# Kernel tuning notes

Hardware: AMD Instinct MI355X
Metric: run time of the kernel (lower is better)

Reference implementation:

```python
import jax, jax.numpy as jnp
import numpy as np

B, N, H = 32, 1024, 256
ALPHA = 0.2  # leaky relu slope
NEG_INF = -1e12


def setup_inputs() -> dict:
    key = jax.random.key(0)
    k1, k2, k3, k4, k5, k6 = jax.random.split(key, 6)
    inp = jax.random.normal(k1, (B, N, H), dtype=jnp.float32)
    A = (jax.random.uniform(k2, (B, N, N)) < 0.05).astype(jnp.float32)
    l = jnp.sort(jax.random.randint(k3, (B, 2), 0, N), axis=1)
    # xavier-uniform(gain=1.414) approximated; exact init values are irrelevant for correctness
    lim_w = 1.414 * np.sqrt(6.0 / (H + H))
    W_i = jax.random.uniform(k4, (H, H), minval=-lim_w, maxval=lim_w, dtype=jnp.float32)
    W_c = jax.random.uniform(k5, (H, H), minval=-lim_w, maxval=lim_w, dtype=jnp.float32)
    lim_a = 1.414 * np.sqrt(6.0 / (2 * H + 1))
    a = jax.random.uniform(k6, (2 * H, 1), minval=-lim_a, maxval=lim_a, dtype=jnp.float32)
    return {"inp": inp, "A": A, "l": l, "W_i": W_i, "W_c": W_c, "a": a}


def reference(inp, A, l, W_i, W_c, a):
    # eval mode: dropout is identity (training=False)
    n = inp.shape[1]
    h = inp.shape[2]
    Wh_i = jnp.einsum('bnh,he->bne', inp, W_i)
    Wh_c = jnp.einsum('bnh,he->bne', inp, W_c)
    # vectorized replacement of the per-batch Wh[index][i:j] = Wh_i[index][i:j] loop
    idx = jnp.arange(n)
    sel = (idx[None, :] >= l[:, 0:1]) & (idx[None, :] < l[:, 1:2])  # [B,N]
    Wh = jnp.where(sel[:, :, None], Wh_i, Wh_c)
    # additive attention scores
    Wh1 = Wh @ a[:h, :]  # [B,N,1]
    Wh2 = Wh @ a[h:, :]  # [B,N,1]
    A_ = A + jnp.eye(n, dtype=A.dtype)
    e = jax.nn.leaky_relu((Wh1 + jnp.swapaxes(Wh2, 1, 2)) * A_, ALPHA)
    att = jnp.where(A_ > 0, e, NEG_INF)
    att = jax.nn.softmax(att, axis=2)
    h_prime = jnp.einsum('bnm,bme->bne', att, Wh)
    return jax.nn.elu(h_prime)  # concat=True
```

## Files before the change

### kernel.cpp

```cpp
#include <hip/hip_runtime.h>
#include <hip/hip_bf16.h>
#include <stdint.h>

#define B_ 32
#define N_ 1024
#define H_ 256
#define PF_PITCH 520

typedef short bf16x8 __attribute__((ext_vector_type(8)));
typedef float floatx4 __attribute__((ext_vector_type(4)));

__device__ inline unsigned short f2bs(float x) {
    __hip_bfloat16 h = __float2bfloat16(x);
    return __builtin_bit_cast(unsigned short, h);
}

__global__ __launch_bounds__(256)
void k_uvec(const float* __restrict__ Wi, const float* __restrict__ Wc,
            const float* __restrict__ a, float* __restrict__ U) {
    int k = blockIdx.x;
    int t = threadIdx.x;
    float wi = Wi[k * H_ + t];
    float wc = Wc[k * H_ + t];
    float a1 = a[t], a2 = a[H_ + t];
    float p0 = wi * a1, p1 = wc * a1, p2 = wi * a2, p3 = wc * a2;
    for (int off = 32; off; off >>= 1) {
        p0 += __shfl_xor(p0, off);
        p1 += __shfl_xor(p1, off);
        p2 += __shfl_xor(p2, off);
        p3 += __shfl_xor(p3, off);
    }
    __shared__ float red[4][4];
    int w = t >> 6;
    if ((t & 63) == 0) { red[w][0] = p0; red[w][1] = p1; red[w][2] = p2; red[w][3] = p3; }
    __syncthreads();
    if (t == 0) {
        U[0 * H_ + k] = red[0][0] + red[1][0] + red[2][0] + red[3][0];
        U[1 * H_ + k] = red[0][1] + red[1][1] + red[2][1] + red[3][1];
        U[2 * H_ + k] = red[0][2] + red[1][2] + red[2][2] + red[3][2];
        U[3 * H_ + k] = red[0][3] + red[1][3] + red[2][3] + red[3][3];
    }
}

__global__ __launch_bounds__(256)
void k_abits(const float* __restrict__ A, unsigned int* __restrict__ M) {
    int t = threadIdx.x, w = t >> 6, lane = t & 63;
    size_t row = blockIdx.x;
    const float* Ar = A + row * N_ + w * 256 + lane * 4;
    float4 v = *reinterpret_cast<const float4*>(Ar);
    unsigned long long b0 = __ballot(v.x > 0.f);
    unsigned long long b1 = __ballot(v.y > 0.f);
    unsigned long long b2 = __ballot(v.z > 0.f);
    unsigned long long b3 = __ballot(v.w > 0.f);
    if (lane == 0) {
        unsigned int* Mp = M + (row * 4 + w) * 8;
        uint4 v0 = {(unsigned int)b0, (unsigned int)(b0 >> 32),
                    (unsigned int)b1, (unsigned int)(b1 >> 32)};
        uint4 v1 = {(unsigned int)b2, (unsigned int)(b2 >> 32),
                    (unsigned int)b3, (unsigned int)(b3 >> 32)};
        *reinterpret_cast<uint4*>(Mp) = v0;
        *reinterpret_cast<uint4*>(Mp + 4) = v1;
    }
}

__global__ __launch_bounds__(256)
void k_prep(const float* __restrict__ Wi, const float* __restrict__ Wc,
            unsigned short* __restrict__ WtFi, unsigned short* __restrict__ WtFc) {
    __shared__ float tile[64][65];
    int mat = blockIdx.x >> 4;
    int tr = ((blockIdx.x >> 2) & 3) * 64;
    int tc = (blockIdx.x & 3) * 64;
    const float* W = mat ? Wc : Wi;
    unsigned short* WtF = mat ? WtFc : WtFi;
    int t = threadIdx.x;
    int rr = t >> 2, c4 = (t & 3) * 16;
    const float* src = W + (size_t)(tr + rr) * H_ + tc + c4;
#pragma unroll
    for (int j = 0; j < 4; ++j) {
        float4 v = *reinterpret_cast<const float4*>(src + j * 4);
        tile[rr][c4 + 4 * j + 0] = v.x;
        tile[rr][c4 + 4 * j + 1] = v.y;
        tile[rr][c4 + 4 * j + 2] = v.z;
        tile[rr][c4 + 4 * j + 3] = v.w;
    }
    __syncthreads();
#pragma unroll
    for (int h = 0; h < 2; ++h) {
        int s = h * 256 + t;
        int ksl = s >> 8;
        int cl  = (s >> 6) & 3;
        int ll  = s & 63;
        int m16v = ll & 15, quadv = ll >> 4;
        int nloc = cl * 16 + m16v;
        int kb = ksl * 32 + quadv * 8;
        unsigned int pk[4];
#pragma unroll
        for (int jj = 0; jj < 4; ++jj) {
            unsigned short lo = f2bs(tile[kb + 2 * jj][nloc]);
            unsigned short hi = f2bs(tile[kb + 2 * jj + 1][nloc]);
            pk[jj] = (unsigned int)lo | ((unsigned int)hi << 16);
        }
        int ksg = (tr >> 5) + ksl;
        int cg  = (tc >> 4) + cl;
        *reinterpret_cast<uint4*>(WtF + ((size_t)(ksg * 16 + cg) * 64 + ll) * 8) =
            *reinterpret_cast<uint4*>(pk);
    }
}

__global__ __launch_bounds__(256)
void k_gemm(const float* __restrict__ inp, const int* __restrict__ l,
            const unsigned short* __restrict__ WtFi, const unsigned short* __restrict__ WtFc,
            unsigned short* __restrict__ WhF, const float* __restrict__ U,
            float* __restrict__ Wh1, float* __restrict__ Wh2) {
    __shared__ unsigned short bbuf[2][4096];
    int blk = blockIdx.x;
    int b  = blk >> 5;
    int r0 = ((blk >> 1) & 15) * 64;
    int n0 = (blk & 1) * 128;
    int t = threadIdx.x;
    int w = t >> 6;
    int lane = t & 63;
    int quad = lane >> 4, m16 = lane & 15;
    int rowb = r0 + w * 16;

    int l0 = l[2 * b], l1 = l[2 * b + 1];
    bool allI = (l0 <= r0) && (r0 + 64 <= l1);
    bool allC = (l1 <= r0) || (l0 >= r0 + 64);
    int npass = (allI || allC) ? 1 : 2;

    int row = rowb + m16;
    bool sel = (row >= l0) && (row < l1);
    const float* xrow = inp + ((size_t)(b * N_ + row)) * H_;
    const float* u1 = U + (sel ? 0 : H_);
    const float* u2 = U + 2 * H_ + (sel ? 0 : H_);
    bool doWh = (n0 == 0);
    float d1 = 0.f, d2 = 0.f;

    unsigned short* fb = WhF + (size_t)b * (N_ * H_);
    int cb = n0 >> 4;

    int j0 = rowb + quad * 4;
    int ksO = j0 >> 5;
    int laneF = m16 + 16 * ((j0 & 31) >> 3);
    int jj0 = j0 & 7;

    for (int pass = 0; pass < npass; ++pass) {
        const unsigned short* WtF =
            (npass == 1) ? (allI ? WtFi : WtFc) : (pass == 0 ? WtFi : WtFc);
        const unsigned short* gbase = WtF + cb * 512;

        floatx4 acc[8];
#pragma unroll
        for (int c = 0; c < 8; ++c) acc[c] = (floatx4){0.f, 0.f, 0.f, 0.f};

        {
            uint4 v0 = *reinterpret_cast<const uint4*>(gbase + (size_t)t * 8);
            uint4 v1 = *reinterpret_cast<const uint4*>(gbase + (size_t)(256 + t) * 8);
            *reinterpret_cast<uint4*>(&bbuf[0][t * 8]) = v0;
            *reinterpret_cast<uint4*>(&bbuf[0][(256 + t) * 8]) = v1;
        }
        for (int ks = 0; ks < 8; ++ks) {
            __syncthreads();
            uint4 v0, v1;
            if (ks < 7) {
                v0 = *reinterpret_cast<const uint4*>(gbase + (size_t)(ks + 1) * 8192 + t * 8);
                v1 = *reinterpret_cast<const uint4*>(gbase + (size_t)(ks + 1) * 8192 + (256 + t) * 8);
            }
            const float4 xa = *reinterpret_cast<const float4*>(xrow + ks * 32 + quad * 8);
            const float4 xb = *reinterpret_cast<const float4*>(xrow + ks * 32 + quad * 8 + 4);
            if (pass == 0 && doWh) {
                const float4 ua = *reinterpret_cast<const float4*>(u1 + ks * 32 + quad * 8);
                const float4 ub = *reinterpret_cast<const float4*>(u1 + ks * 32 + quad * 8 + 4);
                const float4 va = *reinterpret_cast<const float4*>(u2 + ks * 32 + quad * 8);
                const float4 vb = *reinterpret_cast<const float4*>(u2 + ks * 32 + quad * 8 + 4);
                d1 += xa.x * ua.x + xa.y * ua.y + xa.z * ua.z + xa.w * ua.w
                    + xb.x * ub.x + xb.y * ub.y + xb.z * ub.z + xb.w * ub.w;
                d2 += xa.x * va.x + xa.y * va.y + xa.z * va.z + xa.w * va.w
                    + xb.x * vb.x + xb.y * vb.y + xb.z * vb.z + xb.w * vb.w;
            }
            unsigned int pk0 = (unsigned int)f2bs(xa.x) | ((unsigned int)f2bs(xa.y) << 16);
            unsigned int pk1 = (unsigned int)f2bs(xa.z) | ((unsigned int)f2bs(xa.w) << 16);
            unsigned int pk2 = (unsigned int)f2bs(xb.x) | ((unsigned int)f2bs(xb.y) << 16);
            unsigned int pk3 = (unsigned int)f2bs(xb.z) | ((unsigned int)f2bs(xb.w) << 16);
            uint4 apk = {pk0, pk1, pk2, pk3};
            bf16x8 af = __builtin_bit_cast(bf16x8, apk);

            const unsigned short* bptr = &bbuf[ks & 1][lane * 8];
#pragma unroll
            for (int c = 0; c < 8; ++c) {
                bf16x8 bfr = *reinterpret_cast<const bf16x8*>(bptr + c * 512);
                acc[c] = __builtin_amdgcn_mfma_f32_16x16x32_bf16(af, bfr, acc[c], 0, 0, 0);
            }
            if (ks < 7) {
                *reinterpret_cast<uint4*>(&bbuf[(ks + 1) & 1][t * 8]) = v0;
                *reinterpret_cast<uint4*>(&bbuf[(ks + 1) & 1][(256 + t) * 8]) = v1;
            }
        }
        __syncthreads();

#pragma unroll
        for (int c = 0; c < 8; ++c) {
            size_t base = ((size_t)((ksO * 16 + cb + c) * 64) + laneF) * 8 + jj0;
            if (npass == 1) {
                unsigned int lo = (unsigned int)f2bs(acc[c][0]) | ((unsigned int)f2bs(acc[c][1]) << 16);
                unsigned int hi = (unsigned int)f2bs(acc[c][2]) | ((unsigned int)f2bs(acc[c][3]) << 16);
                uint2 v = {lo, hi};
                *reinterpret_cast<uint2*>(fb + base) = v;
            } else {
                bool want[4]; bool all = true, none = true;
#pragma unroll
                for (int r = 0; r < 4; ++r) {
                    int j = j0 + r;
                    bool s2 = (j >= l0) && (j < l1);
                    want[r] = (pass == 0) ? s2 : !s2;
                    all = all && want[r]; none = none && !want[r];
                }
                if (all) {
                    unsigned int lo = (unsigned int)f2bs(acc[c][0]) | ((unsigned int)f2bs(acc[c][1]) << 16);
                    unsigned int hi = (unsigned int)f2bs(acc[c][2]) | ((unsigned int)f2bs(acc[c][3]) << 16);
                    uint2 v = {lo, hi};
                    *reinterpret_cast<uint2*>(fb + base) = v;
                } else if (!none) {
#pragma unroll
                    for (int r = 0; r < 4; ++r)
                        if (want[r]) fb[base + r] = f2bs(acc[c][r]);
                }
            }
        }
    }

    if (doWh) {
        d1 += __shfl_xor(d1, 16); d1 += __shfl_xor(d1, 32);
        d2 += __shfl_xor(d2, 16); d2 += __shfl_xor(d2, 32);
        if (quad == 0) {
            Wh1[b * N_ + rowb + m16] = d1;
            Wh2[b * N_ + rowb + m16] = d2;
        }
    }
}

__global__ __launch_bounds__(256)
void k_attn(const unsigned int* __restrict__ Mask, const float* __restrict__ Wh1,
            const float* __restrict__ Wh2, const unsigned short* __restrict__ WhF,
            float* __restrict__ out) {
    __shared__ unsigned short pfrag[2][32 * PF_PITCH];
    int t = threadIdx.x, w = t >> 6, lane = t & 63;
    int bi = blockIdx.x;
    int b = (bi & 7) * 4 + (bi >> 8);
    int tile = (bi >> 3) & 31;
    int rowbase = tile * 32;

    const float* Wh2b = Wh2 + b * N_;
    float4 w2v[4];
#pragma unroll
    for (int ch = 0; ch < 4; ++ch)
        w2v[ch] = *reinterpret_cast<const float4*>(Wh2b + ch * 256 + lane * 4);

    int ksl = lane >> 3;
    int q2 = (lane >> 1) & 3;
    int jj0 = (lane & 1) * 4;
    int d  = lane >> 5;
    int lb = lane & 31;

#pragma unroll
    for (int tt = 0; tt < 2; ++tt) {
#pragma unroll
        for (int q = 0; q < 4; ++q) {
            int m = w * 4 + q;
            int i = rowbase + tt * 16 + m;
            float wh1 = Wh1[b * N_ + i];
            const uint2* Mrow = reinterpret_cast<const uint2*>(
                Mask + ((size_t)(b * N_ + i)) * 32);
            unsigned int wv[4][4];
#pragma unroll
            for (int ch = 0; ch < 4; ++ch)
#pragma unroll
                for (int c = 0; c < 4; ++c) {
                    uint2 u = Mrow[ch * 4 + c];
                    wv[ch][c] = d ? u.y : u.x;
                }
            int s = m + 16 * q2;
            int sw = s ^ ((s >> 3) & 7);
            int sls = sw * 8 + jj0;
#pragma unroll
            for (int ch = 0; ch < 4; ++ch) {
                float aa[4];
#pragma unroll
                for (int c = 0; c < 4; ++c)
                    aa[c] = (float)((wv[ch][c] >> lb) & 1u);
                if ((i >> 2) == (ch * 64 + lane)) aa[i & 3] += 1.0f;
                float ww[4] = {w2v[ch].x, w2v[ch].y, w2v[ch].z, w2v[ch].w};
                float p[4];
#pragma unroll
                for (int c = 0; c < 4; ++c) {
                    float e  = (wh1 + ww[c]) * aa[c];
                    float lv = fmaxf(e, 0.2f * e);
                    p[c] = aa[c] > 0.f ? __expf(lv) : 0.f;
                }
                unsigned int lo = (unsigned int)f2bs(p[0]) | ((unsigned int)f2bs(p[1]) << 16);
                unsigned int hi = (unsigned int)f2bs(p[2]) | ((unsigned int)f2bs(p[3]) << 16);
                uint2 v = {lo, hi};
                int ks = ch * 8 + ksl;
                *reinterpret_cast<uint2*>(pfrag[tt] + ks * PF_PITCH + sls) = v;
            }
        }
    }
    __syncthreads();

    const unsigned short* WB = WhF + (size_t)b * (N_ * H_);
    int rs = (lane ^ ((lane >> 3) & 7)) * 8;
    unsigned short oneb = f2bs(1.0f);
    bf16x8 bones = {(short)oneb, (short)oneb, (short)oneb, (short)oneb,
                    (short)oneb, (short)oneb, (short)oneb, (short)oneb};
    floatx4 acc0[4], acc1[4], sum0, sum1;
    sum0 = (floatx4){0.f, 0.f, 0.f, 0.f};
    sum1 = (floatx4){0.f, 0.f, 0.f, 0.f};
#pragma unroll
    for (int cc = 0; cc < 4; ++cc) {
        acc0[cc] = (floatx4){0.f, 0.f, 0.f, 0.f};
        acc1[cc] = (floatx4){0.f, 0.f, 0.f, 0.f};
    }
#pragma unroll 2
    for (int ks = 0; ks < 32; ++ks) {
        bf16x8 af0 = *reinterpret_cast<const bf16x8*>(pfrag[0] + ks * PF_PITCH + rs);
        bf16x8 af1 = *reinterpret_cast<const bf16x8*>(pfrag[1] + ks * PF_PITCH + rs);
        sum0 = __builtin_amdgcn_mfma_f32_16x16x32_bf16(af0, bones, sum0, 0, 0, 0);
        sum1 = __builtin_amdgcn_mfma_f32_16x16x32_bf16(af1, bones, sum1, 0, 0, 0);
#pragma unroll
        for (int cc = 0; cc < 4; ++cc) {
            int c = w * 4 + cc;
            bf16x8 bfv = *reinterpret_cast<const bf16x8*>(
                WB + ((size_t)((ks * 16 + c) * 64 + lane)) * 8);
            acc0[cc] = __builtin_amdgcn_mfma_f32_16x16x32_bf16(af0, bfv, acc0[cc], 0, 0, 0);
            acc1[cc] = __builtin_amdgcn_mfma_f32_16x16x32_bf16(af1, bfv, acc1[cc], 0, 0, 0);
        }
    }

    int quad = lane >> 4, m16 = lane & 15;
    float inv0[4], inv1[4];
#pragma unroll
    for (int r = 0; r < 4; ++r) {
        inv0[r] = 1.0f / sum0[r];
        inv1[r] = 1.0f / sum1[r];
    }
#pragma unroll
    for (int cc = 0; cc < 4; ++cc) {
        int col = (w * 4 + cc) * 16 + m16;
#pragma unroll
        for (int r = 0; r < 4; ++r) {
            int m = quad * 4 + r;
            float v0 = acc0[cc][r] * inv0[r];
            v0 = v0 > 0.f ? v0 : __expf(v0) - 1.0f;
            out[((size_t)(b * N_ + rowbase + m)) * H_ + col] = v0;
            float v1 = acc1[cc][r] * inv1[r];
            v1 = v1 > 0.f ? v1 : __expf(v1) - 1.0f;
            out[((size_t)(b * N_ + rowbase + 16 + m)) * H_ + col] = v1;
        }
    }
}

extern "C" void kernel_launch(void* const* d_in, const int* in_sizes, int n_in,
                              void* d_out, int out_size, void* d_ws, size_t ws_size,
                              hipStream_t stream) {
    const float* inp = (const float*)d_in[0];
    const float* A   = (const float*)d_in[1];
    const int*   l   = (const int*)d_in[2];
    const float* Wi  = (const float*)d_in[3];
    const float* Wc  = (const float*)d_in[4];
    const float* a   = (const float*)d_in[5];
    float* out = (float*)d_out;

    char* ws = (char*)d_ws;
    size_t off = 0;
    unsigned short* WhF  = (unsigned short*)(ws + off); off += (size_t)B_ * N_ * H_ * 2;
    float* Wh1 = (float*)(ws + off); off += (size_t)B_ * N_ * 4;
    float* Wh2 = (float*)(ws + off); off += (size_t)B_ * N_ * 4;
    float* U   = (float*)(ws + off); off += 4 * H_ * 4;
    unsigned short* WtFi = (unsigned short*)(ws + off); off += (size_t)H_ * H_ * 2;
    unsigned short* WtFc = (unsigned short*)(ws + off); off += (size_t)H_ * H_ * 2;
    unsigned int* Mask = (unsigned int*)(ws + off); off += (size_t)B_ * N_ * 32 * 4;

    k_abits<<<B_ * N_, 256, 0, stream>>>(A, Mask);
    k_uvec<<<H_, 256, 0, stream>>>(Wi, Wc, a, U);
    k_prep<<<32, 256, 0, stream>>>(Wi, Wc, WtFi, WtFc);
    k_gemm<<<B_ * 16 * 2, 256, 0, stream>>>(inp, l, WtFi, WtFc, WhF, U, Wh1, Wh2);
    k_attn<<<B_ * (N_ / 32), 256, 0, stream>>>(Mask, Wh1, Wh2, WhF, out);
}
```

Before: 294.8 us.

## Merge prep and mask kernels, widen GEMM tile, compute row sums in softmax

Five launches become three. The weight-prep and u-vector kernels merge into one launch, and the adjacency bitmask blocks are folded into the projection GEMM grid as extra blocks. Each GEMM block now covers all 256 output columns, with twice the LDS and accumulators, and computes the attention-score dot products up front. The attention kernel drops the ones-vector MFMA row-sum in favour of a wavefront reduction of the exp values, and adds software prefetch of the A and B fragments. These changes target launch overhead, redundant activation loads and MFMA work, at the cost of fewer GEMM blocks and higher register and LDS pressure.

```diff
diff --git a/kernel.cpp b/kernel.cpp
--- a/kernel.cpp
+++ b/kernel.cpp
@@ -6,6 +6,7 @@
 #define N_ 1024
 #define H_ 256
 #define PF_PITCH 520
+#define GEMM_BLOCKS (B_ * 16)
 
 typedef short bf16x8 __attribute__((ext_vector_type(8)));
 typedef float floatx4 __attribute__((ext_vector_type(4)));
@@ -16,110 +17,109 @@
 }
 
 __global__ __launch_bounds__(256)
-void k_uvec(const float* __restrict__ Wi, const float* __restrict__ Wc,
-            const float* __restrict__ a, float* __restrict__ U) {
-    int k = blockIdx.x;
+void k_pre(const float* __restrict__ Wi, const float* __restrict__ Wc,
+           const float* __restrict__ a, float* __restrict__ U,
+           unsigned short* __restrict__ WtFi, unsigned short* __restrict__ WtFc) {
+    int bid = blockIdx.x;
     int t = threadIdx.x;
-    float wi = Wi[k * H_ + t];
-    float wc = Wc[k * H_ + t];
-    float a1 = a[t], a2 = a[H_ + t];
-    float p0 = wi * a1, p1 = wc * a1, p2 = wi * a2, p3 = wc * a2;
-    for (int off = 32; off; off >>= 1) {
-        p0 += __shfl_xor(p0, off);
-        p1 += __shfl_xor(p1, off);
-        p2 += __shfl_xor(p2, off);
-        p3 += __shfl_xor(p3, off);
-    }
-    __shared__ float red[4][4];
-    int w = t >> 6;
-    if ((t & 63) == 0) { red[w][0] = p0; red[w][1] = p1; red[w][2] = p2; red[w][3] = p3; }
-    __syncthreads();
-    if (t == 0) {
-        U[0 * H_ + k] = red[0][0] + red[1][0] + red[2][0] + red[3][0];
-        U[1 * H_ + k] = red[0][1] + red[1][1] + red[2][1] + red[3][1];
-        U[2 * H_ + k] = red[0][2] + red[1][2] + red[2][2] + red[3][2];
-        U[3 * H_ + k] = red[0][3] + red[1][3] + red[2][3] + red[3][3];
+    if (bid < 32) {
+        __shared__ float tile[64][65];
+        int mat = bid >> 4;
+        int tr = ((bid >> 2) & 3) * 64;
+        int tc = (bid & 3) * 64;
+        const float* W = mat ? Wc : Wi;
+        unsigned short* WtF = mat ? WtFc : WtFi;
+        int rr = t >> 2, c4 = (t & 3) * 16;
+        const float* src = W + (size_t)(tr + rr) * H_ + tc + c4;
+#pragma unroll
+        for (int j = 0; j < 4; ++j) {
+            float4 v = *reinterpret_cast<const float4*>(src + j * 4);
+            tile[rr][c4 + 4 * j + 0] = v.x;
+            tile[rr][c4 + 4 * j + 1] = v.y;
+            tile[rr][c4 + 4 * j + 2] = v.z;
+            tile[rr][c4 + 4 * j + 3] = v.w;
+        }
+        __syncthreads();
+#pragma unroll
+        for (int h = 0; h < 2; ++h) {
+            int s = h * 256 + t;
+            int ksl = s >> 8;
+            int cl  = (s >> 6) & 3;
+            int ll  = s & 63;
+            int m16v = ll & 15, quadv = ll >> 4;
+            int nloc = cl * 16 + m16v;
+            int kb = ksl * 32 + quadv * 8;
+            unsigned int pk[4];
+#pragma unroll
+            for (int jj = 0; jj < 4; ++jj) {
+                unsigned short lo = f2bs(tile[kb + 2 * jj][nloc]);
+                unsigned short hi = f2bs(tile[kb + 2 * jj + 1][nloc]);
+                pk[jj] = (unsigned int)lo | ((unsigned int)hi << 16);
+            }
+            int ksg = (tr >> 5) + ksl;
+            int cg  = (tc >> 4) + cl;
+            *reinterpret_cast<uint4*>(WtF + ((size_t)(ksg * 16 + cg) * 64 + ll) * 8) =
+                *reinterpret_cast<uint4*>(pk);
+        }
+    } else {
+        int k = bid - 32;
+        float wi = Wi[k * H_ + t];
+        float wc = Wc[k * H_ + t];
+        float a1 = a[t], a2 = a[H_ + t];
+        float p0 = wi * a1, p1 = wc * a1, p2 = wi * a2, p3 = wc * a2;
+        for (int off = 32; off; off >>= 1) {
+            p0 += __shfl_xor(p0, off);
+            p1 += __shfl_xor(p1, off);
+            p2 += __shfl_xor(p2, off);
+            p3 += __shfl_xor(p3, off);
+        }
+        __shared__ float red[4][4];
+        int w = t >> 6;
+        if ((t & 63) == 0) { red[w][0] = p0; red[w][1] = p1; red[w][2] = p2; red[w][3] = p3; }
+        __syncthreads();
+        if (t == 0) {
+            U[0 * H_ + k] = red[0][0] + red[1][0] + red[2][0] + red[3][0];
+            U[1 * H_ + k] = red[0][1] + red[1][1] + red[2][1] + red[3][1];
+            U[2 * H_ + k] = red[0][2] + red[1][2] + red[2][2] + red[3][2];
+            U[3 * H_ + k] = red[0][3] + red[1][3] + red[2][3] + red[3][3];
+        }
     }
 }
 
-__global__ __launch_bounds__(256)
-void k_abits(const float* __restrict__ A, unsigned int* __restrict__ M) {
-    int t = threadIdx.x, w = t >> 6, lane = t & 63;
-    size_t row = blockIdx.x;
-    const float* Ar = A + row * N_ + w * 256 + lane * 4;
-    float4 v = *reinterpret_cast<const float4*>(Ar);
-    unsigned long long b0 = __ballot(v.x > 0.f);
-    unsigned long long b1 = __ballot(v.y > 0.f);
-    unsigned long long b2 = __ballot(v.z > 0.f);
-    unsigned long long b3 = __ballot(v.w > 0.f);
-    if (lane == 0) {
-        unsigned int* Mp = M + (row * 4 + w) * 8;
-        uint4 v0 = {(unsigned int)b0, (unsigned int)(b0 >> 32),
-                    (unsigned int)b1, (unsigned int)(b1 >> 32)};
-        uint4 v1 = {(unsigned int)b2, (unsigned int)(b2 >> 32),
-                    (unsigned int)b3, (unsigned int)(b3 >> 32)};
-        *reinterpret_cast<uint4*>(Mp) = v0;
-        *reinterpret_cast<uint4*>(Mp + 4) = v1;
-    }
-}
-
-__global__ __launch_bounds__(256)
-void k_prep(const float* __restrict__ Wi, const float* __restrict__ Wc,
-            unsigned short* __restrict__ WtFi, unsigned short* __restrict__ WtFc) {
-    __shared__ float tile[64][65];
-    int mat = blockIdx.x >> 4;
-    int tr = ((blockIdx.x >> 2) & 3) * 64;
-    int tc = (blockIdx.x & 3) * 64;
-    const float* W = mat ? Wc : Wi;
-    unsigned short* WtF = mat ? WtFc : WtFi;
-    int t = threadIdx.x;
-    int rr = t >> 2, c4 = (t & 3) * 16;
-    const float* src = W + (size_t)(tr + rr) * H_ + tc + c4;
-#pragma unroll
-    for (int j = 0; j < 4; ++j) {
-        float4 v = *reinterpret_cast<const float4*>(src + j * 4);
-        tile[rr][c4 + 4 * j + 0] = v.x;
-        tile[rr][c4 + 4 * j + 1] = v.y;
-        tile[rr][c4 + 4 * j + 2] = v.z;
-        tile[rr][c4 + 4 * j + 3] = v.w;
-    }
-    __syncthreads();
-#pragma unroll
-    for (int h = 0; h < 2; ++h) {
-        int s = h * 256 + t;
-        int ksl = s >> 8;
-        int cl  = (s >> 6) & 3;
-        int ll  = s & 63;
-        int m16v = ll & 15, quadv = ll >> 4;
-        int nloc = cl * 16 + m16v;
-        int kb = ksl * 32 + quadv * 8;
-        unsigned int pk[4];
-#pragma unroll
-        for (int jj = 0; jj < 4; ++jj) {
-            unsigned short lo = f2bs(tile[kb + 2 * jj][nloc]);
-            unsigned short hi = f2bs(tile[kb + 2 * jj + 1][nloc]);
-            pk[jj] = (unsigned int)lo | ((unsigned int)hi << 16);
-        }
-        int ksg = (tr >> 5) + ksl;
-        int cg  = (tc >> 4) + cl;
-        *reinterpret_cast<uint4*>(WtF + ((size_t)(ksg * 16 + cg) * 64 + ll) * 8) =
-            *reinterpret_cast<uint4*>(pk);
-    }
-}
-
-__global__ __launch_bounds__(256)
-void k_gemm(const float* __restrict__ inp, const int* __restrict__ l,
+__global__ __launch_bounds__(256, 2)
+void k_main(const float* __restrict__ inp, const int* __restrict__ l,
             const unsigned short* __restrict__ WtFi, const unsigned short* __restrict__ WtFc,
             unsigned short* __restrict__ WhF, const float* __restrict__ U,
-            float* __restrict__ Wh1, float* __restrict__ Wh2) {
-    __shared__ unsigned short bbuf[2][4096];
-    int blk = blockIdx.x;
-    int b  = blk >> 5;
-    int r0 = ((blk >> 1) & 15) * 64;
-    int n0 = (blk & 1) * 128;
+            float* __restrict__ Wh1, float* __restrict__ Wh2,
+            const float* __restrict__ A, unsigned int* __restrict__ M) {
+    int bid = blockIdx.x;
     int t = threadIdx.x;
     int w = t >> 6;
     int lane = t & 63;
+    if (bid >= GEMM_BLOCKS) {
+        size_t row = bid - GEMM_BLOCKS;
+        const float* Ar = A + row * N_ + w * 256 + lane * 4;
+        float4 v = *reinterpret_cast<const float4*>(Ar);
+        unsigned long long b0 = __ballot(v.x > 0.f);
+        unsigned long long b1 = __ballot(v.y > 0.f);
+        unsigned long long b2 = __ballot(v.z > 0.f);
+        unsigned long long b3 = __ballot(v.w > 0.f);
+        if (lane == 0) {
+            unsigned int* Mp = M + (row * 4 + w) * 8;
+            uint4 v0 = {(unsigned int)b0, (unsigned int)(b0 >> 32),
+                        (unsigned int)b1, (unsigned int)(b1 >> 32)};
+            uint4 v1 = {(unsigned int)b2, (unsigned int)(b2 >> 32),
+                        (unsigned int)b3, (unsigned int)(b3 >> 32)};
+            *reinterpret_cast<uint4*>(Mp) = v0;
+            *reinterpret_cast<uint4*>(Mp + 4) = v1;
+        }
+        return;
+    }
+
+    __shared__ unsigned short bbuf[2][8192];
+    int blk = bid;
+    int b  = blk >> 4;
+    int r0 = (blk & 15) * 64;
     int quad = lane >> 4, m16 = lane & 15;
     int rowb = r0 + w * 16;
 
@@ -133,51 +133,60 @@
     const float* xrow = inp + ((size_t)(b * N_ + row)) * H_;
     const float* u1 = U + (sel ? 0 : H_);
     const float* u2 = U + 2 * H_ + (sel ? 0 : H_);
-    bool doWh = (n0 == 0);
+
     float d1 = 0.f, d2 = 0.f;
+#pragma unroll 2
+    for (int ks = 0; ks < 8; ++ks) {
+        const float4 xa = *reinterpret_cast<const float4*>(xrow + ks * 32 + quad * 8);
+        const float4 xb = *reinterpret_cast<const float4*>(xrow + ks * 32 + quad * 8 + 4);
+        const float4 ua = *reinterpret_cast<const float4*>(u1 + ks * 32 + quad * 8);
+        const float4 ub = *reinterpret_cast<const float4*>(u1 + ks * 32 + quad * 8 + 4);
+        const float4 va = *reinterpret_cast<const float4*>(u2 + ks * 32 + quad * 8);
+        const float4 vb = *reinterpret_cast<const float4*>(u2 + ks * 32 + quad * 8 + 4);
+        d1 += xa.x * ua.x + xa.y * ua.y + xa.z * ua.z + xa.w * ua.w
+            + xb.x * ub.x + xb.y * ub.y + xb.z * ub.z + xb.w * ub.w;
+        d2 += xa.x * va.x + xa.y * va.y + xa.z * va.z + xa.w * va.w
+            + xb.x * vb.x + xb.y * vb.y + xb.z * vb.z + xb.w * vb.w;
+    }
+    d1 += __shfl_xor(d1, 16); d1 += __shfl_xor(d1, 32);
+    d2 += __shfl_xor(d2, 16); d2 += __shfl_xor(d2, 32);
+    if (quad == 0) {
+        Wh1[b * N_ + rowb + m16] = d1;
+        Wh2[b * N_ + rowb + m16] = d2;
+    }
 
     unsigned short* fb = WhF + (size_t)b * (N_ * H_);
-    int cb = n0 >> 4;
-
     int j0 = rowb + quad * 4;
     int ksO = j0 >> 5;
     int laneF = m16 + 16 * ((j0 & 31) >> 3);
     int jj0 = j0 & 7;
 
     for (int pass = 0; pass < npass; ++pass) {
-        const unsigned short* WtF =
+        const unsigned short* gbase =
             (npass == 1) ? (allI ? WtFi : WtFc) : (pass == 0 ? WtFi : WtFc);
-        const unsigned short* gbase = WtF + cb * 512;
-
-        floatx4 acc[8];
-#pragma unroll
-        for (int c = 0; c < 8; ++c) acc[c] = (floatx4){0.f, 0.f, 0.f, 0.f};
+
+        floatx4 acc[16];
+#pragma unroll
+        for (int c = 0; c < 16; ++c) acc[c] = (floatx4){0.f, 0.f, 0.f, 0.f};
 
         {
-            uint4 v0 = *reinterpret_cast<const uint4*>(gbase + (size_t)t * 8);
-            uint4 v1 = *reinterpret_cast<const uint4*>(gbase + (size_t)(256 + t) * 8);
-            *reinterpret_cast<uint4*>(&bbuf[0][t * 8]) = v0;
-            *reinterpret_cast<uint4*>(&bbuf[0][(256 + t) * 8]) = v1;
+            const unsigned short* s0 = gbase + (size_t)t * 32;
+#pragma unroll
+            for (int j = 0; j < 4; ++j)
+                *reinterpret_cast<uint4*>(&bbuf[0][t * 32 + j * 8]) =
+                    *reinterpret_cast<const uint4*>(s0 + j * 8);
         }
         for (int ks = 0; ks < 8; ++ks) {
             __syncthreads();
-            uint4 v0, v1;
+            uint4 v[4];
             if (ks < 7) {
-                v0 = *reinterpret_cast<const uint4*>(gbase + (size_t)(ks + 1) * 8192 + t * 8);
-                v1 = *reinterpret_cast<const uint4*>(gbase + (size_t)(ks + 1) * 8192 + (256 + t) * 8);
+                const unsigned short* sn = gbase + (size_t)(ks + 1) * 8192 + t * 32;
+#pragma unroll
+                for (int j = 0; j < 4; ++j)
+                    v[j] = *reinterpret_cast<const uint4*>(sn + j * 8);
             }
             const float4 xa = *reinterpret_cast<const float4*>(xrow + ks * 32 + quad * 8);
             const float4 xb = *reinterpret_cast<const float4*>(xrow + ks * 32 + quad * 8 + 4);
-            if (pass == 0 && doWh) {
-                const float4 ua = *reinterpret_cast<const float4*>(u1 + ks * 32 + quad * 8);
-                const float4 ub = *reinterpret_cast<const float4*>(u1 + ks * 32 + quad * 8 + 4);
-                const float4 va = *reinterpret_cast<const float4*>(u2 + ks * 32 + quad * 8);
-                const float4 vb = *reinterpret_cast<const float4*>(u2 + ks * 32 + quad * 8 + 4);
-                d1 += xa.x * ua.x + xa.y * ua.y + xa.z * ua.z + xa.w * ua.w
-                    + xb.x * ub.x + xb.y * ub.y + xb.z * ub.z + xb.w * ub.w;
-                d2 += xa.x * va.x + xa.y * va.y + xa.z * va.z + xa.w * va.w
-                    + xb.x * vb.x + xb.y * vb.y + xb.z * vb.z + xb.w * vb.w;
-            }
             unsigned int pk0 = (unsigned int)f2bs(xa.x) | ((unsigned int)f2bs(xa.y) << 16);
             unsigned int pk1 = (unsigned int)f2bs(xa.z) | ((unsigned int)f2bs(xa.w) << 16);
             unsigned int pk2 = (unsigned int)f2bs(xb.x) | ((unsigned int)f2bs(xb.y) << 16);
@@ -187,25 +196,26 @@
 
             const unsigned short* bptr = &bbuf[ks & 1][lane * 8];
 #pragma unroll
-            for (int c = 0; c < 8; ++c) {
+            for (int c = 0; c < 16; ++c) {
                 bf16x8 bfr = *reinterpret_cast<const bf16x8*>(bptr + c * 512);
                 acc[c] = __builtin_amdgcn_mfma_f32_16x16x32_bf16(af, bfr, acc[c], 0, 0, 0);
             }
             if (ks < 7) {
-                *reinterpret_cast<uint4*>(&bbuf[(ks + 1) & 1][t * 8]) = v0;
-                *reinterpret_cast<uint4*>(&bbuf[(ks + 1) & 1][(256 + t) * 8]) = v1;
+#pragma unroll
+                for (int j = 0; j < 4; ++j)
+                    *reinterpret_cast<uint4*>(&bbuf[(ks + 1) & 1][t * 32 + j * 8]) = v[j];
             }
         }
         __syncthreads();
 
 #pragma unroll
-        for (int c = 0; c < 8; ++c) {
-            size_t base = ((size_t)((ksO * 16 + cb + c) * 64) + laneF) * 8 + jj0;
+        for (int c = 0; c < 16; ++c) {
+            size_t base = ((size_t)((ksO * 16 + c) * 64) + laneF) * 8 + jj0;
             if (npass == 1) {
                 unsigned int lo = (unsigned int)f2bs(acc[c][0]) | ((unsigned int)f2bs(acc[c][1]) << 16);
                 unsigned int hi = (unsigned int)f2bs(acc[c][2]) | ((unsigned int)f2bs(acc[c][3]) << 16);
-                uint2 v = {lo, hi};
-                *reinterpret_cast<uint2*>(fb + base) = v;
+                uint2 v2 = {lo, hi};
+                *reinterpret_cast<uint2*>(fb + base) = v2;
             } else {
                 bool want[4]; bool all = true, none = true;
 #pragma unroll
@@ -218,23 +228,14 @@
                 if (all) {
                     unsigned int lo = (unsigned int)f2bs(acc[c][0]) | ((unsigned int)f2bs(acc[c][1]) << 16);
                     unsigned int hi = (unsigned int)f2bs(acc[c][2]) | ((unsigned int)f2bs(acc[c][3]) << 16);
-                    uint2 v = {lo, hi};
-                    *reinterpret_cast<uint2*>(fb + base) = v;
+                    uint2 v2 = {lo, hi};
+                    *reinterpret_cast<uint2*>(fb + base) = v2;
                 } else if (!none) {
 #pragma unroll
                     for (int r = 0; r < 4; ++r)
                         if (want[r]) fb[base + r] = f2bs(acc[c][r]);
                 }
             }
-        }
-    }
-
-    if (doWh) {
-        d1 += __shfl_xor(d1, 16); d1 += __shfl_xor(d1, 32);
-        d2 += __shfl_xor(d2, 16); d2 += __shfl_xor(d2, 32);
-        if (quad == 0) {
-            Wh1[b * N_ + rowb + m16] = d1;
-            Wh2[b * N_ + rowb + m16] = d2;
         }
     }
 }
@@ -244,6 +245,7 @@
             const float* __restrict__ Wh2, const unsigned short* __restrict__ WhF,
             float* __restrict__ out) {
     __shared__ unsigned short pfrag[2][32 * PF_PITCH];
+    __shared__ float rsum[2][16];
     int t = threadIdx.x, w = t >> 6, lane = t & 63;
     int bi = blockIdx.x;
     int b = (bi & 7) * 4 + (bi >> 8);
@@ -282,6 +284,7 @@
             int s = m + 16 * q2;
             int sw = s ^ ((s >> 3) & 7);
             int sls = sw * 8 + jj0;
+            float rp = 0.f;
 #pragma unroll
             for (int ch = 0; ch < 4; ++ch) {
                 float aa[4];
@@ -297,42 +300,53 @@
                     float lv = fmaxf(e, 0.2f * e);
                     p[c] = aa[c] > 0.f ? __expf(lv) : 0.f;
                 }
+                rp += (p[0] + p[1]) + (p[2] + p[3]);
                 unsigned int lo = (unsigned int)f2bs(p[0]) | ((unsigned int)f2bs(p[1]) << 16);
                 unsigned int hi = (unsigned int)f2bs(p[2]) | ((unsigned int)f2bs(p[3]) << 16);
                 uint2 v = {lo, hi};
                 int ks = ch * 8 + ksl;
                 *reinterpret_cast<uint2*>(pfrag[tt] + ks * PF_PITCH + sls) = v;
             }
+            for (int off = 32; off; off >>= 1) rp += __shfl_xor(rp, off);
+            if (lane == 0) rsum[tt][m] = rp;
         }
     }
     __syncthreads();
 
     const unsigned short* WB = WhF + (size_t)b * (N_ * H_);
     int rs = (lane ^ ((lane >> 3) & 7)) * 8;
-    unsigned short oneb = f2bs(1.0f);
-    bf16x8 bones = {(short)oneb, (short)oneb, (short)oneb, (short)oneb,
-                    (short)oneb, (short)oneb, (short)oneb, (short)oneb};
-    floatx4 acc0[4], acc1[4], sum0, sum1;
-    sum0 = (floatx4){0.f, 0.f, 0.f, 0.f};
-    sum1 = (floatx4){0.f, 0.f, 0.f, 0.f};
+    floatx4 acc0[4], acc1[4];
 #pragma unroll
     for (int cc = 0; cc < 4; ++cc) {
         acc0[cc] = (floatx4){0.f, 0.f, 0.f, 0.f};
         acc1[cc] = (floatx4){0.f, 0.f, 0.f, 0.f};
     }
-#pragma unroll 2
+    bf16x8 af0 = *reinterpret_cast<const bf16x8*>(pfrag[0] + rs);
+    bf16x8 af1 = *reinterpret_cast<const bf16x8*>(pfrag[1] + rs);
+    bf16x8 bfv[4];
+#pragma unroll
+    for (int cc = 0; cc < 4; ++cc)
+        bfv[cc] = *reinterpret_cast<const bf16x8*>(
+            WB + ((size_t)((w * 4 + cc) * 64 + lane)) * 8);
     for (int ks = 0; ks < 32; ++ks) {
-        bf16x8 af0 = *reinterpret_cast<const bf16x8*>(pfrag[0] + ks * PF_PITCH + rs);
-        bf16x8 af1 = *reinterpret_cast<const bf16x8*>(pfrag[1] + ks * PF_PITCH + rs);
-        sum0 = __builtin_amdgcn_mfma_f32_16x16x32_bf16(af0, bones, sum0, 0, 0, 0);
-        sum1 = __builtin_amdgcn_mfma_f32_16x16x32_bf16(af1, bones, sum1, 0, 0, 0);
+        bf16x8 naf0, naf1, nbf[4];
+        if (ks < 31) {
+            naf0 = *reinterpret_cast<const bf16x8*>(pfrag[0] + (ks + 1) * PF_PITCH + rs);
+            naf1 = *reinterpret_cast<const bf16x8*>(pfrag[1] + (ks + 1) * PF_PITCH + rs);
+#pragma unroll
+            for (int cc = 0; cc < 4; ++cc)
+                nbf[cc] = *reinterpret_cast<const bf16x8*>(
+                    WB + ((size_t)(((ks + 1) * 16 + w * 4 + cc) * 64 + lane)) * 8);
+        }
 #pragma unroll
         for (int cc = 0; cc < 4; ++cc) {
-            int c = w * 4 + cc;
-            bf16x8 bfv = *reinterpret_cast<const bf16x8*>(
-                WB + ((size_t)((ks * 16 + c) * 64 + lane)) * 8);
-            acc0[cc] = __builtin_amdgcn_mfma_f32_16x16x32_bf16(af0, bfv, acc0[cc], 0, 0, 0);
-            acc1[cc] = __builtin_amdgcn_mfma_f32_16x16x32_bf16(af1, bfv, acc1[cc], 0, 0, 0);
+            acc0[cc] = __builtin_amdgcn_mfma_f32_16x16x32_bf16(af0, bfv[cc], acc0[cc], 0, 0, 0);
+            acc1[cc] = __builtin_amdgcn_mfma_f32_16x16x32_bf16(af1, bfv[cc], acc1[cc], 0, 0, 0);
+        }
+        if (ks < 31) {
+            af0 = naf0; af1 = naf1;
+#pragma unroll
+            for (int cc = 0; cc < 4; ++cc) bfv[cc] = nbf[cc];
         }
     }
 
@@ -340,8 +354,8 @@
     float inv0[4], inv1[4];
 #pragma unroll
     for (int r = 0; r < 4; ++r) {
-        inv0[r] = 1.0f / sum0[r];
-        inv1[r] = 1.0f / sum1[r];
+        inv0[r] = 1.0f / rsum[0][quad * 4 + r];
+        inv1[r] = 1.0f / rsum[1][quad * 4 + r];
     }
 #pragma unroll
     for (int cc = 0; cc < 4; ++cc) {
@@ -380,9 +394,8 @@
     unsigned short* WtFc = (unsigned short*)(ws + off); off += (size_t)H_ * H_ * 2;
     unsigned int* Mask = (unsigned int*)(ws + off); off += (size_t)B_ * N_ * 32 * 4;
 
-    k_abits<<<B_ * N_, 256, 0, stream>>>(A, Mask);
-    k_uvec<<<H_, 256, 0, stream>>>(Wi, Wc, a, U);
-    k_prep<<<32, 256, 0, stream>>>(Wi, Wc, WtFi, WtFc);
-    k_gemm<<<B_ * 16 * 2, 256, 0, stream>>>(inp, l, WtFi, WtFc, WhF, U, Wh1, Wh2);
+    k_pre<<<32 + H_, 256, 0, stream>>>(Wi, Wc, a, U, WtFi, WtFc);
+    k_main<<<GEMM_BLOCKS + B_ * N_, 256, 0, stream>>>(inp, l, WtFi, WtFc, WhF, U,
+                                                      Wh1, Wh2, A, Mask);
     k_attn<<<B_ * (N_ / 32), 256, 0, stream>>>(Mask, Wh1, Wh2, WhF, out);
 }
```

Measured after the change: 310.2 us. 1.05x slower.
